# Optimization experiments

Measured on AMD Instinct MI355X. Metric: run time of the kernel, lower is better.

## Reference

```python
import jax, jax.numpy as jnp
import numpy as np

N = 100000   # product nodes
E = 300000   # edges per relation
DIN = 128    # node_feature_dim
H = 128      # hidden_dim
NEG_SLOPE = 0.2


def setup_inputs() -> dict:
    key = jax.random.key(0)
    ks = iter(jax.random.split(key, 64))
    def nrm(shape, scale):
        return (jax.random.normal(next(ks), shape) * scale).astype(jnp.float32)
    d = {}
    d["x"] = nrm((N, DIN), 1.0)
    d["pos"] = nrm((N, 3), 1.0)
    for name in ("ei_chem", "ei_cond", "ei_mol"):
        d[name] = jax.random.randint(next(ks), (2, E), 0, N, dtype=jnp.int32)
    s = 1.0 / np.sqrt(H)
    d["Wp"] = nrm((DIN, H), 1.0 / np.sqrt(DIN)); d["bp"] = jnp.zeros((H,), jnp.float32)
    for L in ("1", "2"):
        for r in ("c", "d"):  # chemical_transformation, condition_modulation: heads=2
            d[f"W{L}{r}"] = nrm((H, H), s)
            d[f"as{L}{r}"] = nrm((2, H // 2), s)
            d[f"ad{L}{r}"] = nrm((2, H // 2), s)
            d[f"b{L}{r}"] = jnp.zeros((H,), jnp.float32)
        # molecule_target (EQGAT): heads=4
        d[f"W{L}m"] = nrm((H, H), s)
        d[f"as{L}m"] = nrm((4, H // 4), s)
        d[f"ad{L}m"] = nrm((4, H // 4), s)
        d[f"b{L}m"] = jnp.zeros((H,), jnp.float32)
        d[f"Wl{L}"] = nrm((H, H), s)
        d[f"bl{L}"] = jnp.zeros((H,), jnp.float32)
    d["Wy"] = nrm((H, 1), s); d["by"] = jnp.zeros((1,), jnp.float32)
    d["Wa"] = nrm((H, 1), s); d["ba"] = jnp.zeros((1,), jnp.float32)
    return d


def gat_conv(x, row, col, W, a_s, a_d, bias, heads, n):
    """PyG-style GATConv (concat=True, add_self_loops=True)."""
    Fh = W.shape[1] // heads
    loops = jnp.arange(n, dtype=row.dtype)
    row = jnp.concatenate([row, loops])
    col = jnp.concatenate([col, loops])
    h = (x @ W).reshape(n, heads, Fh)                      # [n,Hd,Fh]
    alpha_s = jnp.einsum('nhf,hf->nh', h, a_s)             # [n,Hd]
    alpha_d = jnp.einsum('nhf,hf->nh', h, a_d)
    e = jax.nn.leaky_relu(alpha_s[row] + alpha_d[col], NEG_SLOPE)  # [E',Hd]
    m = jax.lax.stop_gradient(jax.ops.segment_max(e, col, num_segments=n))
    ex = jnp.exp(e - m[col])
    z = jax.ops.segment_sum(ex, col, num_segments=n)
    alpha = ex / (z[col] + 1e-16)                          # per-dst softmax
    msg = h[row] * alpha[:, :, None]                       # [E',Hd,Fh]
    out = jax.ops.segment_sum(msg, col, num_segments=n).reshape(n, heads * Fh)
    return out + bias


def eqgat(x, pos, row, col, W, a_s, a_d, bias, Wl, bl, heads, n):
    geo = jnp.sqrt(jnp.sum((pos[row] - pos[col]) ** 2, axis=-1))  # [E]
    x = x + 0.1 * geo.mean()                                       # scalar broadcast
    h = gat_conv(x, row, col, W, a_s, a_d, bias, heads, n)
    return h @ Wl + bl


def reference(x, pos, ei_chem, ei_cond, ei_mol,
              Wp, bp,
              W1c, as1c, ad1c, b1c, W1d, as1d, ad1d, b1d,
              W1m, as1m, ad1m, b1m, Wl1, bl1,
              W2c, as2c, ad2c, b2c, W2d, as2d, ad2d, b2d,
              W2m, as2m, ad2m, b2m, Wl2, bl2,
              Wy, by, Wa, ba):
    n = x.shape[0]
    h0 = x @ Wp + bp
    h1 = jax.nn.relu(
        gat_conv(h0, ei_chem[0], ei_chem[1], W1c, as1c, ad1c, b1c, 2, n)
        + gat_conv(h0, ei_cond[0], ei_cond[1], W1d, as1d, ad1d, b1d, 2, n)
        + eqgat(h0, pos, ei_mol[0], ei_mol[1], W1m, as1m, ad1m, b1m, Wl1, bl1, 4, n))
    h2 = jax.nn.relu(
        gat_conv(h1, ei_chem[0], ei_chem[1], W2c, as2c, ad2c, b2c, 2, n)
        + gat_conv(h1, ei_cond[0], ei_cond[1], W2d, as2d, ad2d, b2d, 2, n)
        + eqgat(h1, pos, ei_mol[0], ei_mol[1], W2m, as2m, ad2m, b2m, Wl2, bl2, 4, n))
    pred_yield = (h2 @ Wy + by).squeeze(-1)
    pred_activity = (h2 @ Wa + ba).squeeze(-1)
    return jnp.stack([pred_yield, pred_activity], axis=-1)  # [n,2]
```

## Files before the change

kernel.cpp:

```cpp
#include <hip/hip_runtime.h>
#include <math.h>

typedef short short8 __attribute__((ext_vector_type(8)));
typedef float f32x4 __attribute__((ext_vector_type(4)));
typedef unsigned short us4 __attribute__((ext_vector_type(4)));

#define MAXDEG 32
#define GF_BIAS   1
#define GF_CSHIFT 2
#define GF_ALPHA  4
#define NFRAG 18432

__device__ __forceinline__ unsigned short f2bf(float f) {
  unsigned u = __float_as_uint(f);
  u += 0x7FFF + ((u >> 16) & 1);
  return (unsigned short)(u >> 16);
}
__device__ __forceinline__ float bf2f(unsigned short s) { return __uint_as_float(((unsigned)s) << 16); }
__device__ __forceinline__ float lrelu(float v) { return v > 0.f ? v : 0.2f * v; }

__global__ __launch_bounds__(256) void k_scatter3(
    const int* __restrict__ ei0, const int* __restrict__ ei1, const int* __restrict__ ei2,
    int* __restrict__ cur,
    int* __restrict__ s0, int* __restrict__ s1, int* __restrict__ s2,
    const float* __restrict__ pos, float* __restrict__ gsum, int E, int N) {
  __shared__ float part[4];
  const int T4 = gridDim.x * 256;
  const int t = blockIdx.x * 256 + threadIdx.x;
  float d = 0.f;
  #pragma unroll
  for (int k = 0; k < 4; ++k) {
    const int idx = t + k * T4;
    if (idx >= 3 * E) continue;
    int rel, e;
    if (idx < E)          { rel = 0; e = idx; }
    else if (idx < 2 * E) { rel = 1; e = idx - E; }
    else                  { rel = 2; e = idx - 2 * E; }
    const int* ei = (rel == 0) ? ei0 : (rel == 1) ? ei1 : ei2;
    int* srcs     = (rel == 0) ? s0  : (rel == 1) ? s1  : s2;
    const int r = ei[e];
    const int c = ei[E + e];
    const int slot = atomicAdd(&cur[rel * N + c], 1);
    if (slot < MAXDEG) srcs[(size_t)c * MAXDEG + slot] = r;
    if (rel == 2) {
      const float dx = pos[3*r]   - pos[3*c];
      const float dy = pos[3*r+1] - pos[3*c+1];
      const float dz = pos[3*r+2] - pos[3*c+2];
      d += sqrtf(dx*dx + dy*dy + dz*dz);
    }
  }
  #pragma unroll
  for (int o = 32; o; o >>= 1) d += __shfl_down(d, o);
  if ((threadIdx.x & 63) == 0) part[threadIdx.x >> 6] = d;
  __syncthreads();
  if (threadIdx.x == 0) {
    const float s = part[0] + part[1] + part[2] + part[3];
    if (s != 0.f) atomicAdd(gsum, s);
  }
}

struct PrepArgs {
  const float* W[9];
  const float* as_[9];
  const float* ad_[9];
  unsigned short* hi[9];
  unsigned short* lo[9];
  float* csum[9];
  int fh[9];
};

__global__ __launch_bounds__(256) void k_prep(PrepArgs p) {
  const int s = blockIdx.x;
  const int t = threadIdx.x;
  const float* W = p.W[s];
  const int fh = p.fh[s];
  __shared__ float Ws[128 * 129];
  __shared__ float alpha[128 * 8];
  {
    const f32x4* src = (const f32x4*)W;
    for (int i = t; i < 4096; i += 256) {
      const f32x4 v = src[i];
      const int row = i >> 5;
      const int col = (i & 31) * 4;
      float* dst = &Ws[row * 129 + col];
      dst[0] = v[0]; dst[1] = v[1]; dst[2] = v[2]; dst[3] = v[3];
    }
  }
  __syncthreads();
  if (t < 128) {
    #pragma unroll
    for (int a = 0; a < 8; ++a) alpha[t * 8 + a] = 0.f;
    if (fh) {
      const int nh = 128 / fh;
      for (int h = 0; h < nh; ++h) {
        float s1 = 0.f, s2 = 0.f;
        for (int c = 0; c < fh; ++c) {
          const float w = Ws[t * 129 + h * fh + c];
          s1 += w * p.as_[s][h * fh + c];
          s2 += w * p.ad_[s][h * fh + c];
        }
        alpha[t * 8 + h] = s1;
        alpha[t * 8 + 4 + h] = s2;
      }
    }
  }
  __syncthreads();
  for (int idx = t; idx < NFRAG; idx += 256) {
    const int j = idx & 7, lane = (idx >> 3) & 63, kt = (idx >> 9) & 3, nt = idx >> 11;
    const int k = kt * 32 + (lane >> 4) * 8 + j;
    const int col = nt * 16 + (lane & 15);
    float w;
    if (col < 128) w = Ws[k * 129 + col];
    else if (col < 136) w = alpha[k * 8 + (col - 128)];
    else w = 0.f;
    const unsigned short h = f2bf(w);
    p.hi[s][idx] = h;
    p.lo[s][idx] = f2bf(w - bf2f(h));
  }
  if (t < 136) {
    float cs = 0.f;
    if (t < 128) for (int k = 0; k < 128; ++k) cs += Ws[k * 129 + t];
    else         for (int k = 0; k < 128; ++k) cs += alpha[k * 8 + (t - 128)];
    p.csum[s][t] = cs;
  }
}

__global__ __launch_bounds__(256, 2) void k_gmm(
    const float* __restrict__ A, const unsigned short* __restrict__ Whi,
    const unsigned short* __restrict__ Wlo, const float* __restrict__ csum,
    const float* __restrict__ bias, unsigned short* __restrict__ C,
    float* __restrict__ aS, float* __restrict__ aD,
    const float* __restrict__ gsum, float gscale,
    int n, int npad, int flags)
{
  __shared__ unsigned short shi[NFRAG];
  __shared__ unsigned short slo[NFRAG];
  {
    const f32x4* srch = (const f32x4*)Whi;
    const f32x4* srcl = (const f32x4*)Wlo;
    f32x4* dsth = (f32x4*)shi;
    f32x4* dstl = (f32x4*)slo;
    for (int i = threadIdx.x; i < NFRAG / 8; i += 256) { dsth[i] = srch[i]; dstl[i] = srcl[i]; }
  }
  __syncthreads();

  const int wave = threadIdx.x >> 6, lane = threadIdx.x & 63;
  const int m = lane & 15, kq = lane >> 4;
  const float cb = (flags & GF_CSHIFT) ? gscale * gsum[0] : 0.f;

  for (int rb = blockIdx.x * 128; rb < npad; rb += gridDim.x * 128) {
    const int rw = rb + wave * 32;
    short8 ah[2][4], al[2][4];
    #pragma unroll
    for (int sub = 0; sub < 2; ++sub) {
      const int row = rw + sub * 16 + m;
      const bool ok = row < n;
      const float* ap = A + (size_t)row * 128 + kq * 8;
      #pragma unroll
      for (int kt = 0; kt < 4; ++kt) {
        f32x4 x0 = {0.f, 0.f, 0.f, 0.f}, x1 = {0.f, 0.f, 0.f, 0.f};
        if (ok) { x0 = *(const f32x4*)(ap + kt * 32); x1 = *(const f32x4*)(ap + kt * 32 + 4); }
        #pragma unroll
        for (int j = 0; j < 4; ++j) {
          unsigned short h0 = f2bf(x0[j]);
          ah[sub][kt][j] = (short)h0;
          al[sub][kt][j] = (short)f2bf(x0[j] - bf2f(h0));
          unsigned short h1 = f2bf(x1[j]);
          ah[sub][kt][4 + j] = (short)h1;
          al[sub][kt][4 + j] = (short)f2bf(x1[j] - bf2f(h1));
        }
      }
    }
    f32x4 acc[2][9];
    #pragma unroll
    for (int sub = 0; sub < 2; ++sub)
      #pragma unroll
      for (int nt = 0; nt < 9; ++nt) acc[sub][nt] = f32x4{0.f, 0.f, 0.f, 0.f};

    #pragma unroll
    for (int nt = 0; nt < 9; ++nt) {
      #pragma unroll
      for (int kt = 0; kt < 4; ++kt) {
        const int fo = ((nt * 4 + kt) * 64 + lane) * 8;
        const short8 bh = *(const short8*)&shi[fo];
        const short8 bl = *(const short8*)&slo[fo];
        #pragma unroll
        for (int sub = 0; sub < 2; ++sub) {
          acc[sub][nt] = __builtin_amdgcn_mfma_f32_16x16x32_bf16(ah[sub][kt], bh, acc[sub][nt], 0, 0, 0);
          acc[sub][nt] = __builtin_amdgcn_mfma_f32_16x16x32_bf16(al[sub][kt], bh, acc[sub][nt], 0, 0, 0);
          acc[sub][nt] = __builtin_amdgcn_mfma_f32_16x16x32_bf16(ah[sub][kt], bl, acc[sub][nt], 0, 0, 0);
        }
      }
    }
    #pragma unroll
    for (int sub = 0; sub < 2; ++sub) {
      const int rbase = rw + sub * 16 + kq * 4;
      #pragma unroll
      for (int nt = 0; nt < 8; ++nt) {
        const int col = nt * 16 + m;
        const float cs = (flags & GF_CSHIFT) ? cb * csum[col] : 0.f;
        const float bb = (flags & GF_BIAS) ? bias[col] : 0.f;
        #pragma unroll
        for (int r = 0; r < 4; ++r)
          C[(size_t)(rbase + r) * 128 + col] = f2bf(acc[sub][nt][r] + cs + bb);
      }
      if ((flags & GF_ALPHA) && m < 8) {
        const float cs = (flags & GF_CSHIFT) ? cb * csum[128 + m] : 0.f;
        #pragma unroll
        for (int r = 0; r < 4; ++r) {
          const float v = acc[sub][8][r] + cs;
          const int row = rbase + r;
          if (m < 4) aS[(size_t)row * 4 + m] = v;
          else       aD[(size_t)row * 4 + (m - 4)] = v;
        }
      }
    }
  }
}

__global__ __launch_bounds__(256, 2) void k_gmmb(
    const unsigned short* __restrict__ A, const unsigned short* __restrict__ Whi,
    const unsigned short* __restrict__ Wlo, const float* __restrict__ csum,
    const float* __restrict__ bias, unsigned short* __restrict__ C,
    float* __restrict__ aS, float* __restrict__ aD,
    const float* __restrict__ gsum, float gscale,
    int n, int npad, int flags)
{
  __shared__ unsigned short shi[NFRAG];
  __shared__ unsigned short slo[NFRAG];
  {
    const f32x4* srch = (const f32x4*)Whi;
    const f32x4* srcl = (const f32x4*)Wlo;
    f32x4* dsth = (f32x4*)shi;
    f32x4* dstl = (f32x4*)slo;
    for (int i = threadIdx.x; i < NFRAG / 8; i += 256) { dsth[i] = srch[i]; dstl[i] = srcl[i]; }
  }
  __syncthreads();

  const int wave = threadIdx.x >> 6, lane = threadIdx.x & 63;
  const int m = lane & 15, kq = lane >> 4;
  const float cb = (flags & GF_CSHIFT) ? gscale * gsum[0] : 0.f;

  for (int rb = blockIdx.x * 128; rb < npad; rb += gridDim.x * 128) {
    const int rw = rb + wave * 32;
    short8 ah[2][4];
    #pragma unroll
    for (int sub = 0; sub < 2; ++sub) {
      const int row = rw + sub * 16 + m;
      const bool ok = row < n;
      const unsigned short* ap = A + (size_t)row * 128 + kq * 8;
      #pragma unroll
      for (int kt = 0; kt < 4; ++kt) {
        if (ok) ah[sub][kt] = *(const short8*)(ap + kt * 32);
        else    ah[sub][kt] = short8{0, 0, 0, 0, 0, 0, 0, 0};
      }
    }
    f32x4 acc[2][9];
    #pragma unroll
    for (int sub = 0; sub < 2; ++sub)
      #pragma unroll
      for (int nt = 0; nt < 9; ++nt) acc[sub][nt] = f32x4{0.f, 0.f, 0.f, 0.f};

    #pragma unroll
    for (int nt = 0; nt < 9; ++nt) {
      #pragma unroll
      for (int kt = 0; kt < 4; ++kt) {
        const int fo = ((nt * 4 + kt) * 64 + lane) * 8;
        const short8 bh = *(const short8*)&shi[fo];
        const short8 bl = *(const short8*)&slo[fo];
        #pragma unroll
        for (int sub = 0; sub < 2; ++sub) {
          acc[sub][nt] = __builtin_amdgcn_mfma_f32_16x16x32_bf16(ah[sub][kt], bh, acc[sub][nt], 0, 0, 0);
          acc[sub][nt] = __builtin_amdgcn_mfma_f32_16x16x32_bf16(ah[sub][kt], bl, acc[sub][nt], 0, 0, 0);
        }
      }
    }
    #pragma unroll
    for (int sub = 0; sub < 2; ++sub) {
      const int rbase = rw + sub * 16 + kq * 4;
      #pragma unroll
      for (int nt = 0; nt < 8; ++nt) {
        const int col = nt * 16 + m;
        const float cs = (flags & GF_CSHIFT) ? cb * csum[col] : 0.f;
        const float bb = (flags & GF_BIAS) ? bias[col] : 0.f;
        #pragma unroll
        for (int r = 0; r < 4; ++r)
          C[(size_t)(rbase + r) * 128 + col] = f2bf(acc[sub][nt][r] + cs + bb);
      }
      if ((flags & GF_ALPHA) && m < 8) {
        const float cs = (flags & GF_CSHIFT) ? cb * csum[128 + m] : 0.f;
        #pragma unroll
        for (int r = 0; r < 4; ++r) {
          const float v = acc[sub][8][r] + cs;
          const int row = rbase + r;
          if (m < 4) aS[(size_t)row * 4 + m] = v;
          else       aD[(size_t)row * 4 + (m - 4)] = v;
        }
      }
    }
  }
}

__global__ __launch_bounds__(256) void k_conv(
    const unsigned short* __restrict__ hb, const float* __restrict__ aS,
    const float* __restrict__ aD,
    const int* __restrict__ srcs, const int* __restrict__ cnt,
    const float* __restrict__ bias, unsigned short* __restrict__ out,
    int fh_shift, int n)
{
  __shared__ int   ssh[4][2][32];
  __shared__ float wsh[4][2][32][4];
  const int wv = threadIdx.x >> 6;
  const int lane = threadIdx.x & 63;
  const int hf = lane >> 5;
  const int l  = lane & 31;
  const int i = blockIdx.x * 8 + wv * 2 + hf;
  const bool iok = i < n;
  const int ipad = iok ? i : 0;
  const int c0 = l * 4;
  const int hd = c0 >> fh_shift;

  int deg = 0;
  if (iok) { deg = cnt[i]; if (deg > MAXDEG) deg = MAXDEG; }
  const int* sp = srcs + (size_t)ipad * MAXDEG;

  const bool valid = l < deg;
  int s = ipad;
  if (valid) s = sp[l];

  f32x4 ad4 = f32x4{0.f, 0.f, 0.f, 0.f}, asi = f32x4{0.f, 0.f, 0.f, 0.f};
  if (iok) {
    ad4 = *(const f32x4*)(aD + (size_t)i * 4);
    asi = *(const f32x4*)(aS + (size_t)i * 4);
  }
  f32x4 as4 = f32x4{0.f, 0.f, 0.f, 0.f};
  if (valid) as4 = *(const f32x4*)(aS + (size_t)s * 4);

  f32x4 w, z, wsf;
  #pragma unroll
  for (int hh = 0; hh < 4; ++hh) {
    w[hh] = valid ? __expf(lrelu(as4[hh] + ad4[hh])) : 0.f;
    z[hh] = w[hh];
  }
  #pragma unroll
  for (int o = 16; o; o >>= 1) {
    #pragma unroll
    for (int hh = 0; hh < 4; ++hh) z[hh] += __shfl_xor(z[hh], o, 32);
  }
  #pragma unroll
  for (int hh = 0; hh < 4; ++hh) {
    wsf[hh] = __expf(lrelu(asi[hh] + ad4[hh]));
    z[hh] += wsf[hh];
  }

  int dtot = (deg + 3) & ~3;
  const int dmax = max(dtot, __shfl_xor(dtot, 32));
  if (l < dmax) {
    ssh[wv][hf][l] = valid ? s : ipad;
    f32x4 wst = f32x4{0.f, 0.f, 0.f, 0.f};
    if (valid) wst = w;
    *(f32x4*)wsh[wv][hf][l] = wst;
  }

  f32x4 acc = f32x4{0.f, 0.f, 0.f, 0.f};
  {
    us4 u = {0, 0, 0, 0};
    if (iok) u = *(const us4*)(hb + (size_t)i * 128 + c0);
    const float ws = wsf[hd];
    #pragma unroll
    for (int q = 0; q < 4; ++q) acc[q] = ws * bf2f(u[q]);
  }
  for (int j0 = 0; j0 < dmax; j0 += 4) {
    const int s0 = ssh[wv][hf][j0],     s1 = ssh[wv][hf][j0 + 1];
    const int s2 = ssh[wv][hf][j0 + 2], s3 = ssh[wv][hf][j0 + 3];
    const float w0 = wsh[wv][hf][j0][hd],     w1 = wsh[wv][hf][j0 + 1][hd];
    const float w2 = wsh[wv][hf][j0 + 2][hd], w3 = wsh[wv][hf][j0 + 3][hd];
    const us4 u0 = *(const us4*)(hb + (size_t)s0 * 128 + c0);
    const us4 u1 = *(const us4*)(hb + (size_t)s1 * 128 + c0);
    const us4 u2 = *(const us4*)(hb + (size_t)s2 * 128 + c0);
    const us4 u3 = *(const us4*)(hb + (size_t)s3 * 128 + c0);
    #pragma unroll
    for (int q = 0; q < 4; ++q)
      acc[q] += w0 * bf2f(u0[q]) + w1 * bf2f(u1[q]) + w2 * bf2f(u2[q]) + w3 * bf2f(u3[q]);
  }

  if (!iok) return;
  const float inv = 1.f / (z[hd] + 1e-16f);
  const f32x4 bb = *(const f32x4*)(bias + c0);
  unsigned short* op = out + (size_t)i * 128 + c0;
  us4 res;
  #pragma unroll
  for (int q = 0; q < 4; ++q) res[q] = f2bf(acc[q] * inv + bb[q]);
  *(us4*)op = res;
}

__global__ __launch_bounds__(256) void k_conv2(
    const unsigned short* __restrict__ hcp, const unsigned short* __restrict__ hdp,
    const float* __restrict__ aSc, const float* __restrict__ aDc,
    const float* __restrict__ aSd, const float* __restrict__ aDd,
    const int* __restrict__ srcs_c, const int* __restrict__ cnt_c,
    const int* __restrict__ srcs_d, const int* __restrict__ cnt_d,
    const float* __restrict__ bias_c, const float* __restrict__ bias_d,
    unsigned short* __restrict__ out, int n)
{
  __shared__ int   ssh[4][2][2][32];
  __shared__ float wsh[4][2][2][32][2];
  const int wv = threadIdx.x >> 6;
  const int lane = threadIdx.x & 63;
  const int hf = lane >> 5;
  const int l  = lane & 31;
  const int i = blockIdx.x * 8 + wv * 2 + hf;
  const bool iok = i < n;
  const int ipad = iok ? i : 0;
  const int c0 = l * 4;
  const int hd = c0 >> 6;

  const unsigned short* hA[2] = {hcp, hdp};
  const float* aSA[2]  = {aSc, aSd};
  const float* aDA[2]  = {aDc, aDd};
  const int*   spA[2]  = {srcs_c, srcs_d};
  const int*   cntA[2] = {cnt_c, cnt_d};

  int deg[2]; bool valid[2]; int s[2];
  float2 ad2[2], asi2[2], as2[2];
  #pragma unroll
  for (int r = 0; r < 2; ++r) {
    deg[r] = 0;
    if (iok) { int d = cntA[r][i]; deg[r] = d > MAXDEG ? MAXDEG : d; }
  }
  #pragma unroll
  for (int r = 0; r < 2; ++r) {
    const int* sp = spA[r] + (size_t)ipad * MAXDEG;
    valid[r] = l < deg[r];
    s[r] = valid[r] ? sp[l] : ipad;
  }
  #pragma unroll
  for (int r = 0; r < 2; ++r) {
    ad2[r] = float2{0.f, 0.f};
    asi2[r] = float2{0.f, 0.f};
    if (iok) {
      ad2[r] = *(const float2*)(aDA[r] + (size_t)i * 4);
      asi2[r] = *(const float2*)(aSA[r] + (size_t)i * 4);
    }
  }
  #pragma unroll
  for (int r = 0; r < 2; ++r) {
    as2[r] = float2{0.f, 0.f};
    if (valid[r]) as2[r] = *(const float2*)(aSA[r] + (size_t)s[r] * 4);
  }

  float w0_[2], w1_[2], z0_[2], z1_[2], wsf0_[2], wsf1_[2];
  #pragma unroll
  for (int r = 0; r < 2; ++r) {
    w0_[r] = valid[r] ? __expf(lrelu(as2[r].x + ad2[r].x)) : 0.f;
    w1_[r] = valid[r] ? __expf(lrelu(as2[r].y + ad2[r].y)) : 0.f;
    z0_[r] = w0_[r]; z1_[r] = w1_[r];
  }
  #pragma unroll
  for (int o = 16; o; o >>= 1)
    #pragma unroll
    for (int r = 0; r < 2; ++r) {
      z0_[r] += __shfl_xor(z0_[r], o, 32);
      z1_[r] += __shfl_xor(z1_[r], o, 32);
    }
  #pragma unroll
  for (int r = 0; r < 2; ++r) {
    wsf0_[r] = __expf(lrelu(asi2[r].x + ad2[r].x));
    wsf1_[r] = __expf(lrelu(asi2[r].y + ad2[r].y));
    z0_[r] += wsf0_[r];
    z1_[r] += wsf1_[r];
  }

  f32x4 acc = f32x4{0.f, 0.f, 0.f, 0.f};
  #pragma unroll
  for (int rel = 0; rel < 2; ++rel) {
    const float i0 = 1.f / (z0_[rel] + 1e-16f);
    const float i1 = 1.f / (z1_[rel] + 1e-16f);
    int dtot = (deg[rel] + 3) & ~3;
    const int dmax = max(dtot, __shfl_xor(dtot, 32));
    if (l < dmax) {
      ssh[wv][rel][hf][l] = valid[rel] ? s[rel] : ipad;
      float2 wst = float2{0.f, 0.f};
      if (valid[rel]) wst = float2{w0_[rel] * i0, w1_[rel] * i1};
      *(float2*)wsh[wv][rel][hf][l] = wst;
    }

    const unsigned short* hmat = hA[rel];
    {
      us4 u = {0, 0, 0, 0};
      if (iok) u = *(const us4*)(hmat + (size_t)i * 128 + c0);
      const float ws = (hd == 0) ? wsf0_[rel] * i0 : wsf1_[rel] * i1;
      #pragma unroll
      for (int q = 0; q < 4; ++q) acc[q] += ws * bf2f(u[q]);
    }
    for (int j0 = 0; j0 < dmax; j0 += 4) {
      const int s0 = ssh[wv][rel][hf][j0],     s1 = ssh[wv][rel][hf][j0 + 1];
      const int s2 = ssh[wv][rel][hf][j0 + 2], s3 = ssh[wv][rel][hf][j0 + 3];
      const float w0 = wsh[wv][rel][hf][j0][hd],     w1 = wsh[wv][rel][hf][j0 + 1][hd];
      const float w2 = wsh[wv][rel][hf][j0 + 2][hd], w3 = wsh[wv][rel][hf][j0 + 3][hd];
      const us4 u0 = *(const us4*)(hmat + (size_t)s0 * 128 + c0);
      const us4 u1 = *(const us4*)(hmat + (size_t)s1 * 128 + c0);
      const us4 u2 = *(const us4*)(hmat + (size_t)s2 * 128 + c0);
      const us4 u3 = *(const us4*)(hmat + (size_t)s3 * 128 + c0);
      #pragma unroll
      for (int q = 0; q < 4; ++q)
        acc[q] += w0 * bf2f(u0[q]) + w1 * bf2f(u1[q]) + w2 * bf2f(u2[q]) + w3 * bf2f(u3[q]);
    }
  }

  if (!iok) return;
  const f32x4 bbc = *(const f32x4*)(bias_c + c0);
  const f32x4 bbd = *(const f32x4*)(bias_d + c0);
  unsigned short* op = out + (size_t)i * 128 + c0;
  const us4 cu = *(const us4*)op;
  us4 res;
  #pragma unroll
  for (int q = 0; q < 4; ++q)
    res[q] = f2bf(fmaxf(bf2f(cu[q]) + acc[q] + bbc[q] + bbd[q], 0.f));
  *(us4*)op = res;
}

__global__ __launch_bounds__(256) void k_head(
    const unsigned short* __restrict__ h2, const float* __restrict__ Wy,
    const float* __restrict__ by,
    const float* __restrict__ Wa, const float* __restrict__ ba,
    float* __restrict__ out, int n)
{
  const int r = blockIdx.x * 4 + (threadIdx.x >> 6);
  const int L = threadIdx.x & 63;
  if (r >= n) return;
  const float a = bf2f(h2[(size_t)r * 128 + L]);
  const float b = bf2f(h2[(size_t)r * 128 + 64 + L]);
  float py = a * Wy[L] + b * Wy[64 + L];
  float pa = a * Wa[L] + b * Wa[64 + L];
  #pragma unroll
  for (int o = 32; o; o >>= 1) { py += __shfl_down(py, o); pa += __shfl_down(pa, o); }
  if (L == 0) {
    out[(size_t)r * 2]     = py + by[0];
    out[(size_t)r * 2 + 1] = pa + ba[0];
  }
}

extern "C" void kernel_launch(void* const* d_in, const int* in_sizes, int n_in,
                              void* d_out, int out_size, void* d_ws, size_t ws_size,
                              hipStream_t stream) {
  const int N = in_sizes[0] / 128;
  const int E = in_sizes[2] / 2;
  const int npad = (N + 127) & ~127;

  const float* x       = (const float*)d_in[0];
  const float* pos     = (const float*)d_in[1];
  const int*   ei_chem = (const int*)d_in[2];
  const int*   ei_cond = (const int*)d_in[3];
  const int*   ei_mol  = (const int*)d_in[4];
  const float* bp = (const float*)d_in[6];
  const float* Wy = (const float*)d_in[35];
  const float* by = (const float*)d_in[36];
  const float* Wa = (const float*)d_in[37];
  const float* ba = (const float*)d_in[38];

  char* ws = (char*)d_ws;
  size_t off = 0;
  auto alloc = [&](size_t bytes) -> void* {
    void* p = ws + off; off += (bytes + 255) & ~(size_t)255; return p;
  };
  const size_t HBH = (size_t)npad * 128 * sizeof(unsigned short);
  unsigned short* H0b  = (unsigned short*)alloc(HBH);
  unsigned short* ACCb = (unsigned short*)alloc(HBH);
  unsigned short* HRb  = (unsigned short*)alloc(HBH);
  unsigned short* HRb2 = (unsigned short*)alloc(HBH);
  int* SRC[3];
  for (int r = 0; r < 3; ++r) SRC[r] = (int*)alloc((size_t)N * MAXDEG * sizeof(int));
  int*   CUR  = (int*)alloc((size_t)3 * N * sizeof(int));
  float* GSUM = (float*)alloc(256);
  float* AS   = (float*)alloc((size_t)npad * 4 * sizeof(float));
  float* AD   = (float*)alloc((size_t)npad * 4 * sizeof(float));
  float* ASd  = (float*)alloc((size_t)npad * 4 * sizeof(float));
  float* ADd  = (float*)alloc((size_t)npad * 4 * sizeof(float));

  PrepArgs pa{};
  const int widx[9] = {5, 7, 11, 15, 19, 21, 25, 29, 33};
  const int fhs[9]  = {0, 64, 64, 32, 0, 64, 64, 32, 0};
  unsigned short *WHI[9], *WLO[9];
  float* CSUM[9];
  for (int s = 0; s < 9; ++s) {
    WHI[s]  = (unsigned short*)alloc(NFRAG * sizeof(unsigned short));
    WLO[s]  = (unsigned short*)alloc(NFRAG * sizeof(unsigned short));
    CSUM[s] = (float*)alloc(144 * sizeof(float));
    pa.W[s] = (const float*)d_in[widx[s]];
    pa.fh[s] = fhs[s];
    pa.as_[s] = fhs[s] ? (const float*)d_in[widx[s] + 1] : nullptr;
    pa.ad_[s] = fhs[s] ? (const float*)d_in[widx[s] + 2] : nullptr;
    pa.hi[s] = WHI[s]; pa.lo[s] = WLO[s]; pa.csum[s] = CSUM[s];
  }

  hipMemsetAsync(CUR, 0, (size_t)3 * N * sizeof(int), stream);
  hipMemsetAsync(GSUM, 0, sizeof(float), stream);

  {
    const int nthreads = (3 * E + 3) / 4;
    const int sgrid = (nthreads + 255) / 256;
    k_scatter3<<<sgrid, 256, 0, stream>>>(ei_chem, ei_cond, ei_mol,
                                          CUR, SRC[0], SRC[1], SRC[2],
                                          pos, GSUM, E, N);
  }
  k_prep<<<9, 256, 0, stream>>>(pa);

  const int GG = 512;
  const float gscale = 0.1f / (float)E;
  const int cgrid = (N + 7) / 8;

  k_gmm<<<GG, 256, 0, stream>>>(x, WHI[0], WLO[0], CSUM[0], bp, H0b,
                                nullptr, nullptr, nullptr, 0.f, N, npad, GF_BIAS);

  auto layer = [&](const unsigned short* Hin, unsigned short* Acc, int base, int s0) {
    const float* bc = (const float*)d_in[base + 3];
    const float* bd = (const float*)d_in[base + 7];
    const float* bm = (const float*)d_in[base + 11];
    const float* bl = (const float*)d_in[base + 13];
    k_gmmb<<<GG, 256, 0, stream>>>(Hin, WHI[s0+2], WLO[s0+2], CSUM[s0+2], nullptr,
                                   HRb, AS, AD, GSUM, gscale, N, npad,
                                   GF_CSHIFT | GF_ALPHA);
    k_conv<<<cgrid, 256, 0, stream>>>(HRb, AS, AD, SRC[2], CUR + 2*N, bm, Acc, 5, N);
    k_gmmb<<<GG, 256, 0, stream>>>(Acc, WHI[s0+3], WLO[s0+3], CSUM[s0+3], bl, Acc,
                                   nullptr, nullptr, nullptr, 0.f, N, npad, GF_BIAS);
    k_gmmb<<<GG, 256, 0, stream>>>(Hin, WHI[s0+0], WLO[s0+0], CSUM[s0+0], nullptr,
                                   HRb, AS, AD, nullptr, 0.f, N, npad, GF_ALPHA);
    k_gmmb<<<GG, 256, 0, stream>>>(Hin, WHI[s0+1], WLO[s0+1], CSUM[s0+1], nullptr,
                                   HRb2, ASd, ADd, nullptr, 0.f, N, npad, GF_ALPHA);
    k_conv2<<<cgrid, 256, 0, stream>>>(HRb, HRb2, AS, AD, ASd, ADd,
                                       SRC[0], CUR + 0*N, SRC[1], CUR + 1*N,
                                       bc, bd, Acc, N);
  };

  layer(H0b, ACCb, 7, 1);
  layer(ACCb, H0b, 21, 5);

  k_head<<<(N + 3) / 4, 256, 0, stream>>>(H0b, Wy, by, Wa, ba, (float*)d_out, N);
}
```

Before: 656.7 us.

## Interleave chem and cond neighbor gathers in one loop; scatter one edge per thread

The dual-relation GAT aggregation kernel previously walked the chem and cond neighbor lists one after the other. It now stages both lists first, then runs a single loop that issues gathers for both relations together, so more independent global loads are in flight per iteration. Separately, the edge-scatter kernel now assigns one edge per thread with a 4x larger grid instead of four strided edges per thread. The cost is extra registers and predicated zero work when the two degrees differ, plus more blocks and more per-block atomics on the position-distance sum.

```diff
diff --git a/kernel.cpp b/kernel.cpp
--- a/kernel.cpp
+++ b/kernel.cpp
@@ -25,17 +25,13 @@
     int* __restrict__ s0, int* __restrict__ s1, int* __restrict__ s2,
     const float* __restrict__ pos, float* __restrict__ gsum, int E, int N) {
   __shared__ float part[4];
-  const int T4 = gridDim.x * 256;
   const int t = blockIdx.x * 256 + threadIdx.x;
   float d = 0.f;
-  #pragma unroll
-  for (int k = 0; k < 4; ++k) {
-    const int idx = t + k * T4;
-    if (idx >= 3 * E) continue;
+  if (t < 3 * E) {
     int rel, e;
-    if (idx < E)          { rel = 0; e = idx; }
-    else if (idx < 2 * E) { rel = 1; e = idx - E; }
-    else                  { rel = 2; e = idx - 2 * E; }
+    if (t < E)          { rel = 0; e = t; }
+    else if (t < 2 * E) { rel = 1; e = t - E; }
+    else                { rel = 2; e = t - 2 * E; }
     const int* ei = (rel == 0) ? ei0 : (rel == 1) ? ei1 : ei2;
     int* srcs     = (rel == 0) ? s0  : (rel == 1) ? s1  : s2;
     const int r = ei[e];
@@ -46,7 +42,7 @@
       const float dx = pos[3*r]   - pos[3*c];
       const float dy = pos[3*r+1] - pos[3*c+1];
       const float dz = pos[3*r+2] - pos[3*c+2];
-      d += sqrtf(dx*dx + dy*dy + dz*dz);
+      d = sqrtf(dx*dx + dy*dy + dz*dz);
     }
   }
   #pragma unroll
@@ -470,41 +466,71 @@
     z0_[r] += wsf0_[r];
     z1_[r] += wsf1_[r];
   }
-
-  f32x4 acc = f32x4{0.f, 0.f, 0.f, 0.f};
+  float i0_[2], i1_[2];
+  #pragma unroll
+  for (int r = 0; r < 2; ++r) {
+    i0_[r] = 1.f / (z0_[r] + 1e-16f);
+    i1_[r] = 1.f / (z1_[r] + 1e-16f);
+  }
+
+  int dmaxA[2];
   #pragma unroll
   for (int rel = 0; rel < 2; ++rel) {
-    const float i0 = 1.f / (z0_[rel] + 1e-16f);
-    const float i1 = 1.f / (z1_[rel] + 1e-16f);
     int dtot = (deg[rel] + 3) & ~3;
-    const int dmax = max(dtot, __shfl_xor(dtot, 32));
-    if (l < dmax) {
+    dmaxA[rel] = max(dtot, __shfl_xor(dtot, 32));
+    if (l < dmaxA[rel]) {
       ssh[wv][rel][hf][l] = valid[rel] ? s[rel] : ipad;
       float2 wst = float2{0.f, 0.f};
-      if (valid[rel]) wst = float2{w0_[rel] * i0, w1_[rel] * i1};
+      if (valid[rel]) wst = float2{w0_[rel] * i0_[rel], w1_[rel] * i1_[rel]};
       *(float2*)wsh[wv][rel][hf][l] = wst;
     }
-
-    const unsigned short* hmat = hA[rel];
-    {
-      us4 u = {0, 0, 0, 0};
-      if (iok) u = *(const us4*)(hmat + (size_t)i * 128 + c0);
-      const float ws = (hd == 0) ? wsf0_[rel] * i0 : wsf1_[rel] * i1;
-      #pragma unroll
-      for (int q = 0; q < 4; ++q) acc[q] += ws * bf2f(u[q]);
-    }
-    for (int j0 = 0; j0 < dmax; j0 += 4) {
-      const int s0 = ssh[wv][rel][hf][j0],     s1 = ssh[wv][rel][hf][j0 + 1];
-      const int s2 = ssh[wv][rel][hf][j0 + 2], s3 = ssh[wv][rel][hf][j0 + 3];
-      const float w0 = wsh[wv][rel][hf][j0][hd],     w1 = wsh[wv][rel][hf][j0 + 1][hd];
-      const float w2 = wsh[wv][rel][hf][j0 + 2][hd], w3 = wsh[wv][rel][hf][j0 + 3][hd];
-      const us4 u0 = *(const us4*)(hmat + (size_t)s0 * 128 + c0);
-      const us4 u1 = *(const us4*)(hmat + (size_t)s1 * 128 + c0);
-      const us4 u2 = *(const us4*)(hmat + (size_t)s2 * 128 + c0);
-      const us4 u3 = *(const us4*)(hmat + (size_t)s3 * 128 + c0);
-      #pragma unroll
-      for (int q = 0; q < 4; ++q)
-        acc[q] += w0 * bf2f(u0[q]) + w1 * bf2f(u1[q]) + w2 * bf2f(u2[q]) + w3 * bf2f(u3[q]);
+  }
+
+  f32x4 acc = f32x4{0.f, 0.f, 0.f, 0.f};
+  {
+    us4 uc = {0, 0, 0, 0}, ud = {0, 0, 0, 0};
+    if (iok) {
+      uc = *(const us4*)(hcp + (size_t)i * 128 + c0);
+      ud = *(const us4*)(hdp + (size_t)i * 128 + c0);
+    }
+    const float wc = (hd == 0) ? wsf0_[0] * i0_[0] : wsf1_[0] * i1_[0];
+    const float wd = (hd == 0) ? wsf0_[1] * i0_[1] : wsf1_[1] * i1_[1];
+    #pragma unroll
+    for (int q = 0; q < 4; ++q) acc[q] = wc * bf2f(uc[q]) + wd * bf2f(ud[q]);
+  }
+
+  const int dmaxM = max(dmaxA[0], dmaxA[1]);
+  for (int j0 = 0; j0 < dmaxM; j0 += 4) {
+    const bool g0 = j0 < dmaxA[0];
+    const bool g1 = j0 < dmaxA[1];
+    us4 u0a = {0,0,0,0}, u1a = {0,0,0,0}, u2a = {0,0,0,0}, u3a = {0,0,0,0};
+    us4 u0b = {0,0,0,0}, u1b = {0,0,0,0}, u2b = {0,0,0,0}, u3b = {0,0,0,0};
+    float wa0 = 0.f, wa1 = 0.f, wa2 = 0.f, wa3 = 0.f;
+    float wb0 = 0.f, wb1 = 0.f, wb2 = 0.f, wb3 = 0.f;
+    if (g0) {
+      const int s0 = ssh[wv][0][hf][j0],     s1 = ssh[wv][0][hf][j0 + 1];
+      const int s2 = ssh[wv][0][hf][j0 + 2], s3 = ssh[wv][0][hf][j0 + 3];
+      wa0 = wsh[wv][0][hf][j0][hd];     wa1 = wsh[wv][0][hf][j0 + 1][hd];
+      wa2 = wsh[wv][0][hf][j0 + 2][hd]; wa3 = wsh[wv][0][hf][j0 + 3][hd];
+      u0a = *(const us4*)(hcp + (size_t)s0 * 128 + c0);
+      u1a = *(const us4*)(hcp + (size_t)s1 * 128 + c0);
+      u2a = *(const us4*)(hcp + (size_t)s2 * 128 + c0);
+      u3a = *(const us4*)(hcp + (size_t)s3 * 128 + c0);
+    }
+    if (g1) {
+      const int s0 = ssh[wv][1][hf][j0],     s1 = ssh[wv][1][hf][j0 + 1];
+      const int s2 = ssh[wv][1][hf][j0 + 2], s3 = ssh[wv][1][hf][j0 + 3];
+      wb0 = wsh[wv][1][hf][j0][hd];     wb1 = wsh[wv][1][hf][j0 + 1][hd];
+      wb2 = wsh[wv][1][hf][j0 + 2][hd]; wb3 = wsh[wv][1][hf][j0 + 3][hd];
+      u0b = *(const us4*)(hdp + (size_t)s0 * 128 + c0);
+      u1b = *(const us4*)(hdp + (size_t)s1 * 128 + c0);
+      u2b = *(const us4*)(hdp + (size_t)s2 * 128 + c0);
+      u3b = *(const us4*)(hdp + (size_t)s3 * 128 + c0);
+    }
+    #pragma unroll
+    for (int q = 0; q < 4; ++q) {
+      acc[q] += wa0 * bf2f(u0a[q]) + wa1 * bf2f(u1a[q]) + wa2 * bf2f(u2a[q]) + wa3 * bf2f(u3a[q]);
+      acc[q] += wb0 * bf2f(u0b[q]) + wb1 * bf2f(u1b[q]) + wb2 * bf2f(u2b[q]) + wb3 * bf2f(u3b[q]);
     }
   }
 
@@ -597,13 +623,9 @@
   hipMemsetAsync(CUR, 0, (size_t)3 * N * sizeof(int), stream);
   hipMemsetAsync(GSUM, 0, sizeof(float), stream);
 
-  {
-    const int nthreads = (3 * E + 3) / 4;
-    const int sgrid = (nthreads + 255) / 256;
-    k_scatter3<<<sgrid, 256, 0, stream>>>(ei_chem, ei_cond, ei_mol,
-                                          CUR, SRC[0], SRC[1], SRC[2],
-                                          pos, GSUM, E, N);
-  }
+  k_scatter3<<<(3 * E + 255) / 256, 256, 0, stream>>>(ei_chem, ei_cond, ei_mol,
+                                                      CUR, SRC[0], SRC[1], SRC[2],
+                                                      pos, GSUM, E, N);
   k_prep<<<9, 256, 0, stream>>>(pa);
 
   const int GG = 512;
```

Result: no change. 655.1 us (-0.2%).
